# Kernel tuning notes

Measured on AMD Instinct MI355X. Metric: run time of the kernel, lower is better.

Reference implementation:

```python
import jax, jax.numpy as jnp
import numpy as np

B, Q, C = 128, 192, 512   # batch, num_queries (= num_targets per sample), num_classes
COST_CLASS = 1.0
BIG = jnp.float32(1e30)


def _lsap_col4row(cost):
    """Exact linear sum assignment (Jonker-Volgenant shortest augmenting path,
    same algorithm as scipy.optimize.linear_sum_assignment).
    cost: [n, n] float32. Returns col4row[i] = column assigned to row i (int32)."""
    n = cost.shape[0]

    def solve_row(cur_row, state):
        u, v, row4col, col4row = state

        # Dijkstra-like search for the shortest augmenting path from cur_row.
        def dj_cond(s):
            return s[6] < 0  # sink not found yet

        def dj_body(s):
            i, minVal, SR, SC, spc, path, sink = s
            SR = SR.at[i].set(True)
            r = minVal + cost[i] - u[i] - v          # reduced path costs, [n]
            upd = (~SC) & (r < spc)
            path = jnp.where(upd, i, path)
            spc = jnp.where(upd, r, spc)
            masked = jnp.where(SC, BIG, spc)
            j = jnp.argmin(masked).astype(jnp.int32)
            minVal = masked[j]
            SC = SC.at[j].set(True)
            unassigned = row4col[j] < 0
            sink = jnp.where(unassigned, j, jnp.int32(-1))
            i = jnp.where(unassigned, i, row4col[j])
            return i, minVal, SR, SC, spc, path, sink

        init = (jnp.asarray(cur_row, jnp.int32), jnp.float32(0.0),
                jnp.zeros(n, bool), jnp.zeros(n, bool),
                jnp.full(n, BIG, jnp.float32), jnp.zeros(n, jnp.int32),
                jnp.int32(-1))
        _, minVal, SR, SC, spc, path, sink = jax.lax.while_loop(dj_cond, dj_body, init)

        # Dual variable updates.
        u = u.at[cur_row].add(minVal)
        others = SR & (jnp.arange(n) != cur_row)   # assigned rows visited in the search
        u = u + jnp.where(others, minVal - spc[col4row], 0.0)
        v = v - jnp.where(SC, minVal - spc, 0.0)

        # Augment along the stored path from sink back to cur_row.
        def aug_cond(s):
            return ~s[3]

        def aug_body(s):
            j, r4c, c4r, _ = s
            i = path[j]
            r4c = r4c.at[j].set(i)
            nj = c4r[i]
            c4r = c4r.at[i].set(j)
            return nj, r4c, c4r, i == cur_row

        _, row4col, col4row, _ = jax.lax.while_loop(
            aug_cond, aug_body, (sink, row4col, col4row, jnp.bool_(False)))
        return u, v, row4col, col4row

    state = (jnp.zeros(n, jnp.float32), jnp.zeros(n, jnp.float32),
             jnp.full(n, -1, jnp.int32), jnp.full(n, -1, jnp.int32))
    _, _, _, col4row = jax.lax.fori_loop(0, n, solve_row, state)
    return col4row


def _match(predictions, targets):
    """BipartiteMatching: cost[b,q,j] = -softmax(pred)[b,q,targets[b,j]];
    per-sample Hungarian. Returns col4row: [B, Q] (row q matched to target col)."""
    prob = jax.nn.softmax(predictions, axis=-1)            # [B,Q,C]
    tgt = targets.astype(jnp.int32)
    cost = -jax.vmap(lambda p, t: p[:, t])(prob, tgt)      # [B,Q,Q]
    return jax.vmap(_lsap_col4row)(COST_CLASS * cost)      # [B,Q]


def setup_inputs() -> dict:
    key = jax.random.key(0)
    k1, k2 = jax.random.split(key)
    predictions = jax.random.normal(k1, (B, Q, C), dtype=jnp.float32)
    targets = jax.random.randint(k2, (B, Q), 0, C).astype(jnp.int64)
    return {"predictions": predictions, "targets": targets}


def reference(predictions, targets):
    # Matching is done under no_grad in the original module.
    col4row = _match(jax.lax.stop_gradient(predictions), targets)          # [B,Q]
    # Since matching is square, every query is matched; the num_classes fill
    # in the original is always fully overwritten.
    target_classes = jnp.take_along_axis(targets, col4row.astype(targets.dtype), axis=1)
    logp = jax.nn.log_softmax(predictions, axis=-1)                        # [B,Q,C]
    nll = -jnp.take_along_axis(logp, target_classes[..., None].astype(jnp.int32), axis=-1)
    return jnp.mean(nll)  # F.cross_entropy with default mean reduction over B*Q
```

## Files before the change

kernel.cpp:

```cpp
#include <hip/hip_runtime.h>
#include <math.h>


#define BB 128
#define QQ 192
#define CC 512
#define NBIG 1e30f

template<int CTRL>
__device__ __forceinline__ int dpp_mov(int x) {
    return __builtin_amdgcn_update_dpp(x, x, CTRL, 0xf, 0xf, false);
}

__device__ __forceinline__ int readlane_i(int v, int l) {
    return __builtin_amdgcn_readlane(v, l);
}
__device__ __forceinline__ float readlane_f(float v, int l) {
    return __int_as_float(__builtin_amdgcn_readlane(__float_as_int(v), l));
}
__device__ __forceinline__ unsigned umin_(unsigned a, unsigned b) { return a < b ? a : b; }

__device__ __forceinline__ float wave_max64(float x) {
    x = fmaxf(x, __int_as_float(dpp_mov<0x111>(__float_as_int(x))));
    x = fmaxf(x, __int_as_float(dpp_mov<0x112>(__float_as_int(x))));
    x = fmaxf(x, __int_as_float(dpp_mov<0x114>(__float_as_int(x))));
    x = fmaxf(x, __int_as_float(dpp_mov<0x118>(__float_as_int(x))));
    x = fmaxf(x, __int_as_float(dpp_mov<0x142>(__float_as_int(x))));
    x = fmaxf(x, __int_as_float(dpp_mov<0x143>(__float_as_int(x))));
    return __int_as_float(__builtin_amdgcn_readlane(__float_as_int(x), 63));
}
__device__ __forceinline__ float wave_sum64(float x) {
    x += __int_as_float(dpp_mov<0x111>(__float_as_int(x)));
    x += __int_as_float(dpp_mov<0x112>(__float_as_int(x)));
    x += __int_as_float(dpp_mov<0x114>(__float_as_int(x)));
    x += __int_as_float(dpp_mov<0x118>(__float_as_int(x)));
    x += __int_as_float(dpp_mov<0x142>(__float_as_int(x)));
    x += __int_as_float(dpp_mov<0x143>(__float_as_int(x)));
    return __int_as_float(__builtin_amdgcn_readlane(__float_as_int(x), 63));
}

__device__ __forceinline__ unsigned wave_min_pk(unsigned x) {
    x = umin_(x, (unsigned)dpp_mov<0x111>((int)x));
    x = umin_(x, (unsigned)dpp_mov<0x112>((int)x));
    x = umin_(x, (unsigned)dpp_mov<0x114>((int)x));
    x = umin_(x, (unsigned)dpp_mov<0x118>((int)x));
    unsigned a = (unsigned)readlane_i((int)x, 15);
    unsigned b = (unsigned)readlane_i((int)x, 31);
    unsigned c = (unsigned)readlane_i((int)x, 47);
    unsigned d = (unsigned)readlane_i((int)x, 63);
    return umin_(umin_(a, b), umin_(c, d));
}

__device__ __forceinline__ unsigned fkey(float f) {
    unsigned b = __float_as_uint(f);
    return b ^ (((unsigned)((int)b >> 31)) | 0x80000000u);
}

#define GET_I3(a, idx) readlane_i((((idx)>>6)==0) ? a##0 : ((((idx)>>6)==1) ? a##1 : a##2), (idx)&63)
#define GET_F3(a, idx) readlane_f((((idx)>>6)==0) ? a##0 : ((((idx)>>6)==1) ? a##1 : a##2), (idx)&63)
#define SET_I3(a, idx, val) do { const int _s=(idx)>>6, _l=(idx)&63; \
    if (_s==0) { if (lane==_l) a##0=(val); } \
    else if (_s==1) { if (lane==_l) a##1=(val); } \
    else { if (lane==_l) a##2=(val); } } while(0)

__launch_bounds__(256)
__global__ void hungarian_kernel(const float* __restrict__ pred,
                                 const int* __restrict__ targets,
                                 float* __restrict__ ws_part) {
    const int b = blockIdx.x;
    const int lane = threadIdx.x & 63;
    const int wv = threadIdx.x >> 6;

    extern __shared__ float smem[];
    float* cost    = smem;
    float* spc_lds = cost + QQ * QQ;
    float* lse_lds = spc_lds + QQ;
    int*   tgt_lds = (int*)(lse_lds + QQ);

    const int t0 = targets[b * QQ + lane];
    const int t1 = targets[b * QQ + lane + 64];
    const int t2 = targets[b * QQ + lane + 128];
    if (wv == 0) { tgt_lds[lane] = t0; tgt_lds[lane + 64] = t1; tgt_lds[lane + 128] = t2; }

    const float* predb = pred + (size_t)b * QQ * CC;
    {
        const int q0 = wv * 48, q1 = q0 + 48;
        float x[8];
        #pragma unroll
        for (int k = 0; k < 8; k++) x[k] = predb[(size_t)q0 * CC + lane + 64 * k];
        for (int q = q0; q < q1; q++) {
            const float* row = predb + (size_t)q * CC;
            float g0 = row[t0], g1 = row[t1], g2 = row[t2];
            float xn[8];
            if (q + 1 < q1) {
                const float* nrow = row + CC;
                #pragma unroll
                for (int k = 0; k < 8; k++) xn[k] = nrow[lane + 64 * k];
            }
            float mx = x[0];
            #pragma unroll
            for (int k = 1; k < 8; k++) mx = fmaxf(mx, x[k]);
            mx = wave_max64(mx);
            float s = 0.f;
            #pragma unroll
            for (int k = 0; k < 8; k++) s += expf(x[k] - mx);
            s = wave_sum64(s);
            float lse = mx + logf(s);
            if (lane == 0) lse_lds[q] = lse;
            cost[q * QQ + lane]       = -expf(g0 - lse);
            cost[q * QQ + lane + 64]  = -expf(g1 - lse);
            cost[q * QQ + lane + 128] = -expf(g2 - lse);
            #pragma unroll
            for (int k = 0; k < 8; k++) x[k] = xn[k];
        }
    }
    __syncthreads();
    if (wv != 0) return;

    float u0 = 0.f, u1 = 0.f, u2 = 0.f;
    float v0 = 0.f, v1 = 0.f, v2 = 0.f;
    int   c0 = -1, c1 = -1, c2 = -1;
    int   r0 = -1, r1 = -1, r2 = -1;

    for (int cur = 0; cur < QQ; cur++) {
        float spc0 = NBIG, spc1 = NBIG, spc2 = NBIG;
        int   p0 = 0, p1 = 0, p2 = 0;
        int   sc0 = 0, sc1 = 0, sc2 = 0;
        unsigned long long SRm0 = 0, SRm1 = 0, SRm2 = 0;
        int   i = cur;
        float minVal = 0.f;
        int   sink;

        while (true) {
            {
                const int is = i >> 6, il = i & 63;
                if (is == 0)      SRm0 |= 1ull << il;
                else if (is == 1) SRm1 |= 1ull << il;
                else              SRm2 |= 1ull << il;
            }
            const float* crow = cost + i * QQ;
            const float cA = crow[lane];
            const float cB = crow[lane + 64];
            const float cD = crow[lane + 128];
            const float ui = GET_F3(u, i);

            float rA = ((minVal + cA) - ui) - v0;  rA = sc0 ? NBIG : rA;
            if (rA < spc0) { spc0 = rA; p0 = i; }
            float rB = ((minVal + cB) - ui) - v1;  rB = sc1 ? NBIG : rB;
            if (rB < spc1) { spc1 = rB; p1 = i; }
            float rD = ((minVal + cD) - ui) - v2;  rD = sc2 ? NBIG : rD;
            if (rD < spc2) { spc2 = rD; p2 = i; }

            unsigned pkA = sc0 ? 0xFFFFFFFFu : ((fkey(spc0) & 0xFFFFFF00u) | (unsigned)lane);
            unsigned pkB = sc1 ? 0xFFFFFFFFu : ((fkey(spc1) & 0xFFFFFF00u) | (unsigned)(lane + 64));
            unsigned pkD = sc2 ? 0xFFFFFFFFu : ((fkey(spc2) & 0xFFFFFF00u) | (unsigned)(lane + 128));
            const unsigned pk = wave_min_pk(umin_(umin_(pkA, pkB), pkD));
            const int jstar = (int)(pk & 255u);
            const int os = jstar >> 6, ol = jstar & 63;

            minVal = readlane_f(os == 0 ? spc0 : (os == 1 ? spc1 : spc2), ol);
            sc0 |= (jstar == lane);
            sc1 |= (jstar == lane + 64);
            sc2 |= (jstar == lane + 128);
            const int rj = readlane_i(os == 0 ? r0 : (os == 1 ? r1 : r2), ol);
            if (rj < 0) { sink = jstar; break; }
            i = rj;
        }

        u0 += (cur == lane) ? minVal : 0.f;
        u1 += (cur == lane + 64) ? minVal : 0.f;
        u2 += (cur == lane + 128) ? minVal : 0.f;
        spc_lds[lane] = spc0; spc_lds[lane + 64] = spc1; spc_lds[lane + 128] = spc2;
        const int f0 = (int)((SRm0 >> lane) & 1ull);
        const int f1 = (int)((SRm1 >> lane) & 1ull);
        const int f2 = (int)((SRm2 >> lane) & 1ull);
        if (f0 && lane != cur)         u0 += minVal - spc_lds[c0];
        if (f1 && (lane + 64) != cur)  u1 += minVal - spc_lds[c1];
        if (f2 && (lane + 128) != cur) u2 += minVal - spc_lds[c2];
        if (sc0) v0 -= (minVal - spc0);
        if (sc1) v1 -= (minVal - spc1);
        if (sc2) v2 -= (minVal - spc2);

        int j = sink;
        while (true) {
            const int pj = GET_I3(p, j);
            SET_I3(r, j, pj);
            const int nj = GET_I3(c, pj);
            SET_I3(c, pj, j);
            if (pj == cur) break;
            j = nj;
        }
    }

    float part = 0.f;
    {
        const int tc0 = tgt_lds[c0], tc1 = tgt_lds[c1], tc2 = tgt_lds[c2];
        part += lse_lds[lane]       - predb[(size_t)lane * CC + tc0];
        part += lse_lds[lane + 64]  - predb[(size_t)(lane + 64) * CC + tc1];
        part += lse_lds[lane + 128] - predb[(size_t)(lane + 128) * CC + tc2];
    }
    part = wave_sum64(part);
    if (lane == 0) ws_part[b] = part;
}

__launch_bounds__(64)
__global__ void reduce_kernel(const float* __restrict__ ws_part,
                              float* __restrict__ out) {
    int lane = threadIdx.x;
    float s = ws_part[lane] + ws_part[lane + 64];
    s = wave_sum64(s);
    if (lane == 0) out[0] = s / (float)(BB * QQ);
}

extern "C" void kernel_launch(void* const* d_in, const int* in_sizes, int n_in,
                              void* d_out, int out_size, void* d_ws, size_t ws_size,
                              hipStream_t stream) {
    const float* pred = (const float*)d_in[0];
    const int* targets = (const int*)d_in[1];
    float* out = (float*)d_out;
    float* ws = (float*)d_ws;

    const int lds_bytes = (QQ * QQ + 3 * QQ) * (int)sizeof(float);

    hipLaunchKernelGGL(hungarian_kernel, dim3(BB), dim3(256), lds_bytes, stream,
                       pred, targets, ws);
    hipLaunchKernelGGL(reduce_kernel, dim3(1), dim3(64), 0, stream, ws, out);
}
```

Measured before the change: 837.1 us.

## Track running packed-min keys, interleave cost rows, fast-path single-step augmentations

The inner Dijkstra loop now keeps a per-lane running minimum of packed (value, column) keys. Each key is built from the fresh reduced cost plus 1.0 as a positive float, which replaces the sign-fixing key recomputation on every step. The cost matrix is stored with three consecutive columns per lane, so each row fetch is a contiguous per-lane access. A fast path handles searches that finish in one step: it skips the full dual update and the augmentation walk and assigns the row and column directly. The +1.0f key trick assumes reduced costs stay above -1 and drops low mantissa bits, which could change tie-breaking.

```diff
diff --git a/kernel.cpp b/kernel.cpp
--- a/kernel.cpp
+++ b/kernel.cpp
@@ -49,11 +49,6 @@
     unsigned c = (unsigned)readlane_i((int)x, 47);
     unsigned d = (unsigned)readlane_i((int)x, 63);
     return umin_(umin_(a, b), umin_(c, d));
-}
-
-__device__ __forceinline__ unsigned fkey(float f) {
-    unsigned b = __float_as_uint(f);
-    return b ^ (((unsigned)((int)b >> 31)) | 0x80000000u);
 }
 
 #define GET_I3(a, idx) readlane_i((((idx)>>6)==0) ? a##0 : ((((idx)>>6)==1) ? a##1 : a##2), (idx)&63)
@@ -107,9 +102,10 @@
             s = wave_sum64(s);
             float lse = mx + logf(s);
             if (lane == 0) lse_lds[q] = lse;
-            cost[q * QQ + lane]       = -expf(g0 - lse);
-            cost[q * QQ + lane + 64]  = -expf(g1 - lse);
-            cost[q * QQ + lane + 128] = -expf(g2 - lse);
+            float* wp = cost + q * QQ + lane * 3;
+            wp[0] = -expf(g0 - lse);
+            wp[1] = -expf(g1 - lse);
+            wp[2] = -expf(g2 - lse);
             #pragma unroll
             for (int k = 0; k < 8; k++) x[k] = xn[k];
         }
@@ -119,17 +115,20 @@
 
     float u0 = 0.f, u1 = 0.f, u2 = 0.f;
     float v0 = 0.f, v1 = 0.f, v2 = 0.f;
-    int   c0 = -1, c1 = -1, c2 = -1;
-    int   r0 = -1, r1 = -1, r2 = -1;
+    int   xx0 = -1, xx1 = -1, xx2 = -1;
+    int   yy0 = -1, yy1 = -1, yy2 = -1;
+
+    const float* crow_base = cost + lane * 3;
 
     for (int cur = 0; cur < QQ; cur++) {
         float spc0 = NBIG, spc1 = NBIG, spc2 = NBIG;
         int   p0 = 0, p1 = 0, p2 = 0;
+        unsigned kp0 = 0xFFFFFFFFu, kp1 = 0xFFFFFFFFu, kp2 = 0xFFFFFFFFu;
         int   sc0 = 0, sc1 = 0, sc2 = 0;
         unsigned long long SRm0 = 0, SRm1 = 0, SRm2 = 0;
         int   i = cur;
         float minVal = 0.f;
-        int   sink;
+        int   sink, steps = 0;
 
         while (true) {
             {
@@ -138,33 +137,51 @@
                 else if (is == 1) SRm1 |= 1ull << il;
                 else              SRm2 |= 1ull << il;
             }
-            const float* crow = cost + i * QQ;
-            const float cA = crow[lane];
-            const float cB = crow[lane + 64];
-            const float cD = crow[lane + 128];
+            const float* cp = crow_base + i * QQ;
+            const float cA = cp[0], cB = cp[1], cD = cp[2];
             const float ui = GET_F3(u, i);
-
-            float rA = ((minVal + cA) - ui) - v0;  rA = sc0 ? NBIG : rA;
+            const float fs = minVal - ui;
+            const float sv0 = sc0 ? NBIG : fs - v0;
+            const float sv1 = sc1 ? NBIG : fs - v1;
+            const float sv2 = sc2 ? NBIG : fs - v2;
+
+            const float rA = cA + sv0;
+            const float rB = cB + sv1;
+            const float rD = cD + sv2;
             if (rA < spc0) { spc0 = rA; p0 = i; }
-            float rB = ((minVal + cB) - ui) - v1;  rB = sc1 ? NBIG : rB;
             if (rB < spc1) { spc1 = rB; p1 = i; }
-            float rD = ((minVal + cD) - ui) - v2;  rD = sc2 ? NBIG : rD;
             if (rD < spc2) { spc2 = rD; p2 = i; }
-
-            unsigned pkA = sc0 ? 0xFFFFFFFFu : ((fkey(spc0) & 0xFFFFFF00u) | (unsigned)lane);
-            unsigned pkB = sc1 ? 0xFFFFFFFFu : ((fkey(spc1) & 0xFFFFFF00u) | (unsigned)(lane + 64));
-            unsigned pkD = sc2 ? 0xFFFFFFFFu : ((fkey(spc2) & 0xFFFFFF00u) | (unsigned)(lane + 128));
-            const unsigned pk = wave_min_pk(umin_(umin_(pkA, pkB), pkD));
+            const unsigned krA = (__float_as_uint(rA + 1.0f) & 0xFFFFFF00u) | (unsigned)lane;
+            const unsigned krB = (__float_as_uint(rB + 1.0f) & 0xFFFFFF00u) | (unsigned)(lane + 64);
+            const unsigned krD = (__float_as_uint(rD + 1.0f) & 0xFFFFFF00u) | (unsigned)(lane + 128);
+            kp0 = umin_(kp0, krA);
+            kp1 = umin_(kp1, krB);
+            kp2 = umin_(kp2, krD);
+
+            const unsigned pk = wave_min_pk(umin_(umin_(kp0, kp1), kp2));
             const int jstar = (int)(pk & 255u);
             const int os = jstar >> 6, ol = jstar & 63;
 
             minVal = readlane_f(os == 0 ? spc0 : (os == 1 ? spc1 : spc2), ol);
+            kp0 = (jstar == lane)       ? 0xFFFFFFFFu : kp0;
+            kp1 = (jstar == lane + 64)  ? 0xFFFFFFFFu : kp1;
+            kp2 = (jstar == lane + 128) ? 0xFFFFFFFFu : kp2;
             sc0 |= (jstar == lane);
             sc1 |= (jstar == lane + 64);
             sc2 |= (jstar == lane + 128);
-            const int rj = readlane_i(os == 0 ? r0 : (os == 1 ? r1 : r2), ol);
+            const int rj = readlane_i(os == 0 ? yy0 : (os == 1 ? yy1 : yy2), ol);
+            steps++;
             if (rj < 0) { sink = jstar; break; }
             i = rj;
+        }
+
+        if (steps == 1) {
+            u0 += (cur == lane) ? minVal : 0.f;
+            u1 += (cur == lane + 64) ? minVal : 0.f;
+            u2 += (cur == lane + 128) ? minVal : 0.f;
+            SET_I3(yy, sink, cur);
+            SET_I3(xx, cur, sink);
+            continue;
         }
 
         u0 += (cur == lane) ? minVal : 0.f;
@@ -174,9 +191,9 @@
         const int f0 = (int)((SRm0 >> lane) & 1ull);
         const int f1 = (int)((SRm1 >> lane) & 1ull);
         const int f2 = (int)((SRm2 >> lane) & 1ull);
-        if (f0 && lane != cur)         u0 += minVal - spc_lds[c0];
-        if (f1 && (lane + 64) != cur)  u1 += minVal - spc_lds[c1];
-        if (f2 && (lane + 128) != cur) u2 += minVal - spc_lds[c2];
+        if (f0 && lane != cur)         u0 += minVal - spc_lds[xx0];
+        if (f1 && (lane + 64) != cur)  u1 += minVal - spc_lds[xx1];
+        if (f2 && (lane + 128) != cur) u2 += minVal - spc_lds[xx2];
         if (sc0) v0 -= (minVal - spc0);
         if (sc1) v1 -= (minVal - spc1);
         if (sc2) v2 -= (minVal - spc2);
@@ -184,9 +201,9 @@
         int j = sink;
         while (true) {
             const int pj = GET_I3(p, j);
-            SET_I3(r, j, pj);
-            const int nj = GET_I3(c, pj);
-            SET_I3(c, pj, j);
+            SET_I3(yy, j, pj);
+            const int nj = GET_I3(xx, pj);
+            SET_I3(xx, pj, j);
             if (pj == cur) break;
             j = nj;
         }
@@ -194,7 +211,7 @@
 
     float part = 0.f;
     {
-        const int tc0 = tgt_lds[c0], tc1 = tgt_lds[c1], tc2 = tgt_lds[c2];
+        const int tc0 = tgt_lds[xx0], tc1 = tgt_lds[xx1], tc2 = tgt_lds[xx2];
         part += lse_lds[lane]       - predb[(size_t)lane * CC + tc0];
         part += lse_lds[lane + 64]  - predb[(size_t)(lane + 64) * CC + tc1];
         part += lse_lds[lane + 128] - predb[(size_t)(lane + 128) * CC + tc2];
```

Result: slower. 859.2 us (+2.6%).

## Collapse duplicate target classes into capacitated columns in the assignment solver

Applied to the files above, without the earlier changes.

Targets that share a class give identical cost columns, so the kernel deduplicates classes into distinct columns, each with a capacity equal to its multiplicity, and runs a capacitated shortest-augmenting-path search over those columns. All rows assigned to a selected column are expanded together, two at a time, which cuts the number of serial Dijkstra steps and wave reductions. The min-key trick now adds 1.0 to the (non-positive) reduced cost instead of flipping sign bits. It adds LDS-atomic setup and a 300-round escape cap that could change results if ever hit, and the cost still comes out equal only because tied classes are interchangeable.

```diff
diff --git a/kernel.cpp b/kernel.cpp
--- a/kernel.cpp
+++ b/kernel.cpp
@@ -51,11 +51,6 @@
     return umin_(umin_(a, b), umin_(c, d));
 }
 
-__device__ __forceinline__ unsigned fkey(float f) {
-    unsigned b = __float_as_uint(f);
-    return b ^ (((unsigned)((int)b >> 31)) | 0x80000000u);
-}
-
 #define GET_I3(a, idx) readlane_i((((idx)>>6)==0) ? a##0 : ((((idx)>>6)==1) ? a##1 : a##2), (idx)&63)
 #define GET_F3(a, idx) readlane_f((((idx)>>6)==0) ? a##0 : ((((idx)>>6)==1) ? a##1 : a##2), (idx)&63)
 #define SET_I3(a, idx, val) do { const int _s=(idx)>>6, _l=(idx)&63; \
@@ -72,15 +67,49 @@
     const int wv = threadIdx.x >> 6;
 
     extern __shared__ float smem[];
-    float* cost    = smem;
-    float* spc_lds = cost + QQ * QQ;
-    float* lse_lds = spc_lds + QQ;
-    int*   tgt_lds = (int*)(lse_lds + QQ);
+    float* cost     = smem;
+    float* spc_lds  = cost + QQ * QQ;
+    float* lse_lds  = spc_lds + QQ;
+    int*   classd   = (int*)(lse_lds + QQ);
+    int*   capd     = classd + QQ;
+    int*   dorig    = capd + QQ;
+    unsigned* tabf  = (unsigned*)(dorig + QQ);
+    unsigned* tabc  = tabf + CC;
 
     const int t0 = targets[b * QQ + lane];
     const int t1 = targets[b * QQ + lane + 64];
     const int t2 = targets[b * QQ + lane + 128];
-    if (wv == 0) { tgt_lds[lane] = t0; tgt_lds[lane + 64] = t1; tgt_lds[lane + 128] = t2; }
+
+    if (wv == 0) {
+        #pragma unroll
+        for (int k = 0; k < 8; k++) { tabf[lane + 64 * k] = 0xFFFFFFFFu; tabc[lane + 64 * k] = 0u; }
+        __threadfence_block();
+        atomicMin(&tabf[t0], (unsigned)lane);
+        atomicMin(&tabf[t1], (unsigned)(lane + 64));
+        atomicMin(&tabf[t2], (unsigned)(lane + 128));
+        atomicAdd(&tabc[t0], 1u);
+        atomicAdd(&tabc[t1], 1u);
+        atomicAdd(&tabc[t2], 1u);
+        __threadfence_block();
+        const unsigned fo0 = tabf[t0], fo1 = tabf[t1], fo2 = tabf[t2];
+        const int isf0 = (fo0 == (unsigned)lane);
+        const int isf1 = (fo1 == (unsigned)(lane + 64));
+        const int isf2 = (fo2 == (unsigned)(lane + 128));
+        const unsigned long long F0 = __ballot(isf0), F1 = __ballot(isf1), F2 = __ballot(isf2);
+        const unsigned long long below = (1ull << lane) - 1ull;
+        const int n0 = __popcll(F0), n1 = __popcll(F1);
+        const int d0 = isf0 ? __popcll(F0 & below) : -1;
+        const int d1 = isf1 ? n0 + __popcll(F1 & below) : -1;
+        const int d2 = isf2 ? n0 + n1 + __popcll(F2 & below) : -1;
+        dorig[lane] = d0; dorig[lane + 64] = d1; dorig[lane + 128] = d2;
+        if (isf0) { classd[d0] = t0; capd[d0] = (int)tabc[t0]; }
+        if (isf1) { classd[d1] = t1; capd[d1] = (int)tabc[t1]; }
+        if (isf2) { classd[d2] = t2; capd[d2] = (int)tabc[t2]; }
+        const int Dtot = n0 + n1 + __popcll(F2);
+        for (int d = Dtot + lane; d < QQ; d += 64) { capd[d] = 0; classd[d] = 0; }
+    }
+    __syncthreads();
+    const int dd0 = dorig[lane], dd1 = dorig[lane + 64], dd2 = dorig[lane + 128];
 
     const float* predb = pred + (size_t)b * QQ * CC;
     {
@@ -107,9 +136,9 @@
             s = wave_sum64(s);
             float lse = mx + logf(s);
             if (lane == 0) lse_lds[q] = lse;
-            cost[q * QQ + lane]       = -expf(g0 - lse);
-            cost[q * QQ + lane + 64]  = -expf(g1 - lse);
-            cost[q * QQ + lane + 128] = -expf(g2 - lse);
+            if (dd0 >= 0) cost[q * QQ + dd0] = -expf(g0 - lse);
+            if (dd1 >= 0) cost[q * QQ + dd1] = -expf(g1 - lse);
+            if (dd2 >= 0) cost[q * QQ + dd2] = -expf(g2 - lse);
             #pragma unroll
             for (int k = 0; k < 8; k++) x[k] = xn[k];
         }
@@ -119,82 +148,119 @@
 
     float u0 = 0.f, u1 = 0.f, u2 = 0.f;
     float v0 = 0.f, v1 = 0.f, v2 = 0.f;
-    int   c0 = -1, c1 = -1, c2 = -1;
-    int   r0 = -1, r1 = -1, r2 = -1;
+    int   xx0 = -1, xx1 = -1, xx2 = -1;
+    const int cap0 = capd[lane], cap1 = capd[lane + 64], cap2 = capd[lane + 128];
+    const int dead0 = (cap0 == 0), dead1 = (cap1 == 0), dead2 = (cap2 == 0);
+    int lf0 = 0, lf1 = 0, lf2 = 0;
+    int fb0 = !dead0, fb1 = !dead1, fb2 = !dead2;
 
     for (int cur = 0; cur < QQ; cur++) {
         float spc0 = NBIG, spc1 = NBIG, spc2 = NBIG;
         int   p0 = 0, p1 = 0, p2 = 0;
-        int   sc0 = 0, sc1 = 0, sc2 = 0;
+        int   sc0 = dead0, sc1 = dead1, sc2 = dead2;
         unsigned long long SRm0 = 0, SRm1 = 0, SRm2 = 0;
-        int   i = cur;
+        unsigned long long P0 = 0, P1 = 0, P2 = 0;
+        {
+            const int cs = cur >> 6, cl = cur & 63;
+            if (cs == 0) P0 = 1ull << cl; else if (cs == 1) P1 = 1ull << cl; else P2 = 1ull << cl;
+        }
         float minVal = 0.f;
-        int   sink;
+        int   sink = -1, rounds = 0;
 
         while (true) {
-            {
-                const int is = i >> 6, il = i & 63;
-                if (is == 0)      SRm0 |= 1ull << il;
-                else if (is == 1) SRm1 |= 1ull << il;
-                else              SRm2 |= 1ull << il;
+            while (P0 | P1 | P2) {
+                int i0;
+                if (P0)      { i0 = __ffsll(P0) - 1;       P0 &= P0 - 1; }
+                else if (P1) { i0 = 64 + __ffsll(P1) - 1;  P1 &= P1 - 1; }
+                else         { i0 = 128 + __ffsll(P2) - 1; P2 &= P2 - 1; }
+                int i1 = -1;
+                if (P0)      { i1 = __ffsll(P0) - 1;       P0 &= P0 - 1; }
+                else if (P1) { i1 = 64 + __ffsll(P1) - 1;  P1 &= P1 - 1; }
+                else if (P2) { i1 = 128 + __ffsll(P2) - 1; P2 &= P2 - 1; }
+
+                const float* q0p = cost + i0 * QQ;
+                const float ca0 = q0p[lane], cb0 = q0p[lane + 64], cc0 = q0p[lane + 128];
+                float ca1, cb1, cc1;
+                if (i1 >= 0) {
+                    const float* q1p = cost + i1 * QQ;
+                    ca1 = q1p[lane]; cb1 = q1p[lane + 64]; cc1 = q1p[lane + 128];
+                }
+                {
+                    const int is = i0 >> 6, il = i0 & 63;
+                    if (is == 0) SRm0 |= 1ull << il; else if (is == 1) SRm1 |= 1ull << il; else SRm2 |= 1ull << il;
+                }
+                if (i1 >= 0) {
+                    const int is = i1 >> 6, il = i1 & 63;
+                    if (is == 0) SRm0 |= 1ull << il; else if (is == 1) SRm1 |= 1ull << il; else SRm2 |= 1ull << il;
+                }
+                const float fs0 = minVal - GET_F3(u, i0);
+                const float sa0 = sc0 ? NBIG : fs0 - v0;
+                const float sb0 = sc1 ? NBIG : fs0 - v1;
+                const float sd0 = sc2 ? NBIG : fs0 - v2;
+                {
+                    float r = ca0 + sa0; if (r < spc0) { spc0 = r; p0 = i0; }
+                    r = cb0 + sb0;       if (r < spc1) { spc1 = r; p1 = i0; }
+                    r = cc0 + sd0;       if (r < spc2) { spc2 = r; p2 = i0; }
+                }
+                if (i1 >= 0) {
+                    const float fs1 = minVal - GET_F3(u, i1);
+                    const float sa1 = sc0 ? NBIG : fs1 - v0;
+                    const float sb1 = sc1 ? NBIG : fs1 - v1;
+                    const float sd1 = sc2 ? NBIG : fs1 - v2;
+                    float r = ca1 + sa1; if (r < spc0) { spc0 = r; p0 = i1; }
+                    r = cb1 + sb1;       if (r < spc1) { spc1 = r; p1 = i1; }
+                    r = cc1 + sd1;       if (r < spc2) { spc2 = r; p2 = i1; }
+                }
             }
-            const float* crow = cost + i * QQ;
-            const float cA = crow[lane];
-            const float cB = crow[lane + 64];
-            const float cD = crow[lane + 128];
-            const float ui = GET_F3(u, i);
-
-            float rA = ((minVal + cA) - ui) - v0;  rA = sc0 ? NBIG : rA;
-            if (rA < spc0) { spc0 = rA; p0 = i; }
-            float rB = ((minVal + cB) - ui) - v1;  rB = sc1 ? NBIG : rB;
-            if (rB < spc1) { spc1 = rB; p1 = i; }
-            float rD = ((minVal + cD) - ui) - v2;  rD = sc2 ? NBIG : rD;
-            if (rD < spc2) { spc2 = rD; p2 = i; }
-
-            unsigned pkA = sc0 ? 0xFFFFFFFFu : ((fkey(spc0) & 0xFFFFFF00u) | (unsigned)lane);
-            unsigned pkB = sc1 ? 0xFFFFFFFFu : ((fkey(spc1) & 0xFFFFFF00u) | (unsigned)(lane + 64));
-            unsigned pkD = sc2 ? 0xFFFFFFFFu : ((fkey(spc2) & 0xFFFFFF00u) | (unsigned)(lane + 128));
-            const unsigned pk = wave_min_pk(umin_(umin_(pkA, pkB), pkD));
-            const int jstar = (int)(pk & 255u);
-            const int os = jstar >> 6, ol = jstar & 63;
-
+
+            const unsigned kp0 = sc0 ? 0xFFFFFFFFu : ((__float_as_uint(spc0 + 1.0f) & 0xFFFFFF00u) | (unsigned)lane);
+            const unsigned kp1 = sc1 ? 0xFFFFFFFFu : ((__float_as_uint(spc1 + 1.0f) & 0xFFFFFF00u) | (unsigned)(lane + 64));
+            const unsigned kp2 = sc2 ? 0xFFFFFFFFu : ((__float_as_uint(spc2 + 1.0f) & 0xFFFFFF00u) | (unsigned)(lane + 128));
+            const unsigned pk = wave_min_pk(umin_(umin_(kp0, kp1), kp2));
+            const int j = (int)(pk & 255u);
+            const int os = j >> 6, ol = j & 63;
             minVal = readlane_f(os == 0 ? spc0 : (os == 1 ? spc1 : spc2), ol);
-            sc0 |= (jstar == lane);
-            sc1 |= (jstar == lane + 64);
-            sc2 |= (jstar == lane + 128);
-            const int rj = readlane_i(os == 0 ? r0 : (os == 1 ? r1 : r2), ol);
-            if (rj < 0) { sink = jstar; break; }
-            i = rj;
+            sc0 |= (j == lane); sc1 |= (j == lane + 64); sc2 |= (j == lane + 128);
+            const int jfree = readlane_i(os == 0 ? fb0 : (os == 1 ? fb1 : fb2), ol);
+            if (jfree || ++rounds > 300) { sink = j; break; }
+            P0 = __ballot(xx0 == j); P1 = __ballot(xx1 == j); P2 = __ballot(xx2 == j);
         }
 
         u0 += (cur == lane) ? minVal : 0.f;
         u1 += (cur == lane + 64) ? minVal : 0.f;
         u2 += (cur == lane + 128) ? minVal : 0.f;
         spc_lds[lane] = spc0; spc_lds[lane + 64] = spc1; spc_lds[lane + 128] = spc2;
-        const int f0 = (int)((SRm0 >> lane) & 1ull);
-        const int f1 = (int)((SRm1 >> lane) & 1ull);
-        const int f2 = (int)((SRm2 >> lane) & 1ull);
-        if (f0 && lane != cur)         u0 += minVal - spc_lds[c0];
-        if (f1 && (lane + 64) != cur)  u1 += minVal - spc_lds[c1];
-        if (f2 && (lane + 128) != cur) u2 += minVal - spc_lds[c2];
-        if (sc0) v0 -= (minVal - spc0);
-        if (sc1) v1 -= (minVal - spc1);
-        if (sc2) v2 -= (minVal - spc2);
-
-        int j = sink;
+        const int g0b = (int)((SRm0 >> lane) & 1ull);
+        const int g1b = (int)((SRm1 >> lane) & 1ull);
+        const int g2b = (int)((SRm2 >> lane) & 1ull);
+        if (g0b && lane != cur)         u0 += minVal - spc_lds[xx0];
+        if (g1b && (lane + 64) != cur)  u1 += minVal - spc_lds[xx1];
+        if (g2b && (lane + 128) != cur) u2 += minVal - spc_lds[xx2];
+        if (sc0 && !dead0) v0 -= (minVal - spc0);
+        if (sc1 && !dead1) v1 -= (minVal - spc1);
+        if (sc2 && !dead2) v2 -= (minVal - spc2);
+
+        {
+            const int sl = sink & 63, ss = sink >> 6;
+            if (lane == sl) {
+                if (ss == 0)      { lf0++; fb0 = lf0 < cap0; }
+                else if (ss == 1) { lf1++; fb1 = lf1 < cap1; }
+                else              { lf2++; fb2 = lf2 < cap2; }
+            }
+        }
+        int j2 = sink;
         while (true) {
-            const int pj = GET_I3(p, j);
-            SET_I3(r, j, pj);
-            const int nj = GET_I3(c, pj);
-            SET_I3(c, pj, j);
+            const int pj = GET_I3(p, j2);
+            const int jold = GET_I3(xx, pj);
+            SET_I3(xx, pj, j2);
             if (pj == cur) break;
-            j = nj;
+            j2 = jold;
         }
     }
 
     float part = 0.f;
     {
-        const int tc0 = tgt_lds[c0], tc1 = tgt_lds[c1], tc2 = tgt_lds[c2];
+        const int tc0 = classd[xx0], tc1 = classd[xx1], tc2 = classd[xx2];
         part += lse_lds[lane]       - predb[(size_t)lane * CC + tc0];
         part += lse_lds[lane + 64]  - predb[(size_t)(lane + 64) * CC + tc1];
         part += lse_lds[lane + 128] - predb[(size_t)(lane + 128) * CC + tc2];
@@ -220,7 +286,9 @@
     float* out = (float*)d_out;
     float* ws = (float*)d_ws;
 
-    const int lds_bytes = (QQ * QQ + 3 * QQ) * (int)sizeof(float);
+    const int lds_bytes = (QQ * QQ + 2 * QQ) * (int)sizeof(float)
+                        + 3 * QQ * (int)sizeof(int)
+                        + 2 * CC * (int)sizeof(unsigned);
 
     hipLaunchKernelGGL(hungarian_kernel, dim3(BB), dim3(256), lds_bytes, stream,
                        pred, targets, ws);
```

Measured after the change: 1.152 ms. +37.7%, slower.

## Speculatively prefetch next Dijkstra cost row using second-minimum column

Applied to the files above, without the earlier changes.

The wave reduction now tracks both the minimum and the second-smallest packed key. Each iteration it prefetches the cost row of the row assigned to the runner-up column, on the guess that the next step will pick it. When the guess matches, the LDS load latency on the serial critical path is hidden. This costs a heavier reduction (two DPP streams, with the row_bcast steps replacing the readlane tail) and an extra row load every iteration.

```diff
diff --git a/kernel.cpp b/kernel.cpp
--- a/kernel.cpp
+++ b/kernel.cpp
@@ -19,6 +19,7 @@
     return __int_as_float(__builtin_amdgcn_readlane(__float_as_int(v), l));
 }
 __device__ __forceinline__ unsigned umin_(unsigned a, unsigned b) { return a < b ? a : b; }
+__device__ __forceinline__ unsigned umax_(unsigned a, unsigned b) { return a > b ? a : b; }
 
 __device__ __forceinline__ float wave_max64(float x) {
     x = fmaxf(x, __int_as_float(dpp_mov<0x111>(__float_as_int(x))));
@@ -39,16 +40,16 @@
     return __int_as_float(__builtin_amdgcn_readlane(__float_as_int(x), 63));
 }
 
-__device__ __forceinline__ unsigned wave_min_pk(unsigned x) {
-    x = umin_(x, (unsigned)dpp_mov<0x111>((int)x));
-    x = umin_(x, (unsigned)dpp_mov<0x112>((int)x));
-    x = umin_(x, (unsigned)dpp_mov<0x114>((int)x));
-    x = umin_(x, (unsigned)dpp_mov<0x118>((int)x));
-    unsigned a = (unsigned)readlane_i((int)x, 15);
-    unsigned b = (unsigned)readlane_i((int)x, 31);
-    unsigned c = (unsigned)readlane_i((int)x, 47);
-    unsigned d = (unsigned)readlane_i((int)x, 63);
-    return umin_(umin_(a, b), umin_(c, d));
+__device__ __forceinline__ void wave_minsub_pk(unsigned& mn, unsigned& sb) {
+#define MSU(CTRL) { \
+    unsigned omn = (unsigned)dpp_mov<CTRL>((int)mn); \
+    unsigned osb = (unsigned)dpp_mov<CTRL>((int)sb); \
+    unsigned lo = umin_(mn, omn), hi = umax_(mn, omn); \
+    mn = lo; sb = umin_(umin_(sb, osb), hi); }
+    MSU(0x111) MSU(0x112) MSU(0x114) MSU(0x118) MSU(0x142) MSU(0x143)
+#undef MSU
+    mn = (unsigned)readlane_i((int)mn, 63);
+    sb = (unsigned)readlane_i((int)sb, 63);
 }
 
 __device__ __forceinline__ unsigned fkey(float f) {
@@ -119,8 +120,8 @@
 
     float u0 = 0.f, u1 = 0.f, u2 = 0.f;
     float v0 = 0.f, v1 = 0.f, v2 = 0.f;
-    int   c0 = -1, c1 = -1, c2 = -1;
-    int   r0 = -1, r1 = -1, r2 = -1;
+    int   xx0 = -1, xx1 = -1, xx2 = -1;
+    int   yy0 = -1, yy1 = -1, yy2 = -1;
 
     for (int cur = 0; cur < QQ; cur++) {
         float spc0 = NBIG, spc1 = NBIG, spc2 = NBIG;
@@ -130,6 +131,9 @@
         int   i = cur;
         float minVal = 0.f;
         int   sink;
+        int   fast = 0;
+        unsigned pred2 = 0xFFFFFFFFu;
+        float pfA = 0.f, pfB = 0.f, pfD = 0.f;
 
         while (true) {
             {
@@ -138,10 +142,23 @@
                 else if (is == 1) SRm1 |= 1ull << il;
                 else              SRm2 |= 1ull << il;
             }
-            const float* crow = cost + i * QQ;
-            const float cA = crow[lane];
-            const float cB = crow[lane + 64];
-            const float cD = crow[lane + 128];
+            int gn = -3;
+            if (pred2 != 0xFFFFFFFFu) {
+                const int j2 = (int)(pred2 & 255u);
+                gn = GET_I3(yy, j2);
+            }
+            float cA, cB, cD;
+            if (fast) {
+                cA = pfA; cB = pfB; cD = pfD;
+            } else {
+                const float* crow = cost + i * QQ;
+                cA = crow[lane]; cB = crow[lane + 64]; cD = crow[lane + 128];
+            }
+            {
+                const int gl = (gn >= 0) ? gn : 0;
+                const float* gp = cost + gl * QQ;
+                pfA = gp[lane]; pfB = gp[lane + 64]; pfD = gp[lane + 128];
+            }
             const float ui = GET_F3(u, i);
 
             float rA = ((minVal + cA) - ui) - v0;  rA = sc0 ? NBIG : rA;
@@ -151,20 +168,26 @@
             float rD = ((minVal + cD) - ui) - v2;  rD = sc2 ? NBIG : rD;
             if (rD < spc2) { spc2 = rD; p2 = i; }
 
-            unsigned pkA = sc0 ? 0xFFFFFFFFu : ((fkey(spc0) & 0xFFFFFF00u) | (unsigned)lane);
-            unsigned pkB = sc1 ? 0xFFFFFFFFu : ((fkey(spc1) & 0xFFFFFF00u) | (unsigned)(lane + 64));
-            unsigned pkD = sc2 ? 0xFFFFFFFFu : ((fkey(spc2) & 0xFFFFFF00u) | (unsigned)(lane + 128));
-            const unsigned pk = wave_min_pk(umin_(umin_(pkA, pkB), pkD));
-            const int jstar = (int)(pk & 255u);
+            const unsigned pkA = sc0 ? 0xFFFFFFFFu : ((fkey(spc0) & 0xFFFFFF00u) | (unsigned)lane);
+            const unsigned pkB = sc1 ? 0xFFFFFFFFu : ((fkey(spc1) & 0xFFFFFF00u) | (unsigned)(lane + 64));
+            const unsigned pkD = sc2 ? 0xFFFFFFFFu : ((fkey(spc2) & 0xFFFFFF00u) | (unsigned)(lane + 128));
+            const unsigned lo = umin_(pkA, pkB), hi = umax_(pkA, pkB);
+            unsigned mn = umin_(lo, pkD);
+            unsigned sb = umin_(hi, umax_(lo, pkD));
+            wave_minsub_pk(mn, sb);
+
+            const int jstar = (int)(mn & 255u);
             const int os = jstar >> 6, ol = jstar & 63;
 
             minVal = readlane_f(os == 0 ? spc0 : (os == 1 ? spc1 : spc2), ol);
             sc0 |= (jstar == lane);
             sc1 |= (jstar == lane + 64);
             sc2 |= (jstar == lane + 128);
-            const int rj = readlane_i(os == 0 ? r0 : (os == 1 ? r1 : r2), ol);
+            const int rj = readlane_i(os == 0 ? yy0 : (os == 1 ? yy1 : yy2), ol);
             if (rj < 0) { sink = jstar; break; }
+            fast = (rj == gn);
             i = rj;
+            pred2 = sb;
         }
 
         u0 += (cur == lane) ? minVal : 0.f;
@@ -174,9 +197,9 @@
         const int f0 = (int)((SRm0 >> lane) & 1ull);
         const int f1 = (int)((SRm1 >> lane) & 1ull);
         const int f2 = (int)((SRm2 >> lane) & 1ull);
-        if (f0 && lane != cur)         u0 += minVal - spc_lds[c0];
-        if (f1 && (lane + 64) != cur)  u1 += minVal - spc_lds[c1];
-        if (f2 && (lane + 128) != cur) u2 += minVal - spc_lds[c2];
+        if (f0 && lane != cur)         u0 += minVal - spc_lds[xx0];
+        if (f1 && (lane + 64) != cur)  u1 += minVal - spc_lds[xx1];
+        if (f2 && (lane + 128) != cur) u2 += minVal - spc_lds[xx2];
         if (sc0) v0 -= (minVal - spc0);
         if (sc1) v1 -= (minVal - spc1);
         if (sc2) v2 -= (minVal - spc2);
@@ -184,9 +207,9 @@
         int j = sink;
         while (true) {
             const int pj = GET_I3(p, j);
-            SET_I3(r, j, pj);
-            const int nj = GET_I3(c, pj);
-            SET_I3(c, pj, j);
+            SET_I3(yy, j, pj);
+            const int nj = GET_I3(xx, pj);
+            SET_I3(xx, pj, j);
             if (pj == cur) break;
             j = nj;
         }
@@ -194,7 +217,7 @@
 
     float part = 0.f;
     {
-        const int tc0 = tgt_lds[c0], tc1 = tgt_lds[c1], tc2 = tgt_lds[c2];
+        const int tc0 = tgt_lds[xx0], tc1 = tgt_lds[xx1], tc2 = tgt_lds[xx2];
         part += lse_lds[lane]       - predb[(size_t)lane * CC + tc0];
         part += lse_lds[lane + 64]  - predb[(size_t)(lane + 64) * CC + tc1];
         part += lse_lds[lane + 128] - predb[(size_t)(lane + 128) * CC + tc2];
```

Result: slower. 1.108 ms (+32.4%).
